# Performance work log

Hardware: AMD Instinct MI355X
Metric: run time of the kernel (lower is better)

Reference implementation:

```python
import jax, jax.numpy as jnp
import numpy as np

N_HEADS = 16
ROPE_THETA = 10000.0


def _rope(x):
    # x: (b, h, t, d). Interleaved-pair rotary embedding (lucidrains
    # rotary_embedding_torch convention: rotate_half on (d r) pairs, r=2).
    b, h, t, d = x.shape
    inv_freq = 1.0 / (ROPE_THETA ** (jnp.arange(0, d, 2, dtype=jnp.float32) / d))  # (d/2,)
    ang = jnp.arange(t, dtype=jnp.float32)[:, None] * inv_freq[None, :]            # (t, d/2)
    cos = jnp.cos(ang)
    sin = jnp.sin(ang)
    xp = x.reshape(b, h, t, d // 2, 2)
    x1, x2 = xp[..., 0], xp[..., 1]
    o1 = x1 * cos - x2 * sin
    o2 = x1 * sin + x2 * cos
    return jnp.stack([o1, o2], axis=-1).reshape(b, h, t, d)


def setup_inputs() -> dict:
    key = jax.random.key(0)
    k1, k2, k3 = jax.random.split(key, 3)
    B, T, C = 4, 2048, 1024
    x = jax.random.normal(k1, (B, T, C), dtype=jnp.float32)
    # torch nn.Linear weight layout: (out_features, in_features)
    w_attn = jax.random.normal(k2, (3 * C, C), dtype=jnp.float32) * (1.0 / np.sqrt(C))
    w_proj = jax.random.normal(k3, (C, C), dtype=jnp.float32) * (1.0 / np.sqrt(C))
    return {"x": x, "w_attn": w_attn, "w_proj": w_proj}


def reference(x, w_attn, w_proj):
    B, T, C = x.shape
    H = N_HEADS
    D = C // H
    # fused QKV projection: (b, t, 3C)
    qkv = jnp.einsum('btc,fc->btf', x, w_attn)
    # rearrange 'b t (r h d) -> r b h t d'
    qkv = qkv.reshape(B, T, 3, H, D).transpose(2, 0, 3, 1, 4)
    q, k, v = qkv[0], qkv[1], qkv[2]
    q = _rope(q)
    k = _rope(k)
    scale = 1.0 / np.sqrt(D).astype(np.float32)
    scores = jnp.einsum('bhqd,bhkd->bhqk', q, k) * scale
    attn = jax.nn.softmax(scores, axis=-1)
    y = jnp.einsum('bhqk,bhkd->bhqd', attn, v)       # (b, h, t, d)
    y = y.transpose(0, 2, 1, 3).reshape(B, T, C)     # 'b h t d -> b t (h d)'
    return jnp.einsum('btc,oc->bto', y, w_proj)
```

## Files before the change

kernel.cpp:

```cpp
#include <hip/hip_runtime.h>
#include <hip/hip_bf16.h>
#include <math.h>

typedef __bf16 bf16;
typedef float f32x4 __attribute__((ext_vector_type(4)));
typedef float f32x16 __attribute__((ext_vector_type(16)));
typedef bf16 bf16x8 __attribute__((ext_vector_type(8)));
typedef bf16 bf16x4 __attribute__((ext_vector_type(4)));
typedef unsigned int uint;
typedef uint uintx2 __attribute__((ext_vector_type(2)));

#define MFMA16(a, b, c) __builtin_amdgcn_mfma_f32_16x16x32_bf16(a, b, c, 0, 0, 0)
#define MFMA32(a, b, c) __builtin_amdgcn_mfma_f32_32x32x16_bf16(a, b, c, 0, 0, 0)

static constexpr int T_SEQ = 2048;
static constexpr int CDIM  = 1024;
static constexpr int NH    = 16;
static constexpr int DH    = 64;
static constexpr float FREQ_C = 0.20762050593045998f;
static constexpr float Q_SCALE = 0.18033688011112042f;

__device__ __forceinline__ float fexp2(float x) {
    return __builtin_amdgcn_exp2f(x);
}

__device__ __forceinline__ uint pack_bf16(float lo, float hi) {
    union { bf16 h[2]; uint u; } cv;
    cv.h[0] = (bf16)lo;
    cv.h[1] = (bf16)hi;
    return cv.u;
}

__device__ __forceinline__ void gld_lds16(const bf16* g, bf16* l) {
    __builtin_amdgcn_global_load_lds(
        (const __attribute__((address_space(1))) void*)g,
        (__attribute__((address_space(3))) void*)l, 16, 0, 0);
}

__device__ __forceinline__ void fast_sincos(float x, float* s, float* c) {
    const float INV2PI = 0.15915494309189535f;
    const float PI2_HI = 6.28125f;
    const float PI2_LO = 1.9353071795864769e-3f;
    const float n = rintf(x * INV2PI);
    float r = fmaf(-n, PI2_HI, x);
    r = fmaf(-n, PI2_LO, r);
    *s = __sinf(r);
    *c = __cosf(r);
}

__device__ __forceinline__ void cvt8(const float* __restrict__ in,
                                     bf16* __restrict__ out, int i) {
    const f32x4* p = (const f32x4*)(in + (size_t)i * 8);
    const f32x4 lo = p[0], hi = p[1];
    bf16x8 o;
    o[0] = (bf16)lo[0]; o[1] = (bf16)lo[1]; o[2] = (bf16)lo[2]; o[3] = (bf16)lo[3];
    o[4] = (bf16)hi[0]; o[5] = (bf16)hi[1]; o[6] = (bf16)hi[2]; o[7] = (bf16)hi[3];
    *(bf16x8*)(out + (size_t)i * 8) = o;
}

__global__ __launch_bounds__(256)
void prologue(const float* __restrict__ x, const float* __restrict__ wa,
              const float* __restrict__ wp, bf16* __restrict__ Xb,
              bf16* __restrict__ Wab, bf16* __restrict__ Wpb,
              float2* __restrict__ tab) {
    const int b = blockIdx.x, tid = threadIdx.x;
    if (b < 4096) {
        cvt8(x, Xb, b * 256 + tid);
    } else if (b < 5632) {
        cvt8(wa, Wab, (b - 4096) * 256 + tid);
    } else if (b < 6144) {
        cvt8(wp, Wpb, (b - 5632) * 256 + tid);
    } else {
        const int i = (b - 6144) * 256 + tid;
        const int t = i >> 5, p = i & 31;
        const float ang = (float)t * exp2f(-2.0f * (float)p * FREQ_C);
        float s, c;
        fast_sincos(ang, &s, &c);
        tab[i] = make_float2(c, s);
    }
}

#define GEMM_CORE(Abase, Bbase, KDIM)                                            \
    f32x4 acc[4][4] = {};                                                        \
    for (int kk = 0; kk < (KDIM); kk += 64) {                                    \
        __syncthreads();                                                         \
        _Pragma("unroll")                                                        \
        for (int u = 0; u < 4; u++) {                                            \
            const int st = wave * 4 + u, mg = st >> 1, kg = st & 1;              \
            gld_lds16(Abase + (size_t)(mg * 16 + sm) * (KDIM) + kk + kg * 32 + sc * 8, \
                      &ash[st * 512]);                                           \
            gld_lds16(Bbase + (size_t)(mg * 16 + sm) * (KDIM) + kk + kg * 32 + sc * 8, \
                      &bsh[st * 512]);                                           \
        }                                                                        \
        __syncthreads();                                                         \
        _Pragma("unroll")                                                        \
        for (int kg = 0; kg < 2; kg++) {                                         \
            bf16x8 af[4], bfr[4];                                                \
            _Pragma("unroll")                                                    \
            for (int a = 0; a < 4; a++)                                          \
                af[a] = *(const bf16x8*)&ash[((wm * 4 + a) * 2 + kg) * 512 + lane * 8]; \
            _Pragma("unroll")                                                    \
            for (int b = 0; b < 4; b++)                                          \
                bfr[b] = *(const bf16x8*)&bsh[((wn * 4 + b) * 2 + kg) * 512 + lane * 8]; \
            _Pragma("unroll")                                                    \
            for (int a = 0; a < 4; a++)                                          \
                _Pragma("unroll")                                                \
                for (int b = 0; b < 4; b++)                                      \
                    acc[a][b] = MFMA16(af[a], bfr[b], acc[a][b]);                \
        }                                                                        \
    }

__global__ __launch_bounds__(256)
void gemm_qkv(const bf16* __restrict__ X, const bf16* __restrict__ W,
              bf16* __restrict__ Qo, bf16* __restrict__ Ko, bf16* __restrict__ Vt,
              const float2* __restrict__ tab) {
    __shared__ __align__(16) bf16 ash[16 * 512];
    __shared__ __align__(16) bf16 bsh[16 * 512];
    const int tid = threadIdx.x, lane = tid & 63, wave = tid >> 6;
    const int quad = lane >> 4, l16 = lane & 15;
    const int wm = wave >> 1, wn = wave & 1;
    const int lin = blockIdx.y * 24 + blockIdx.x;
    const int xcd = lin & 7, j = lin >> 3;
    const int bm = xcd * 8 + (j & 7), bn = j >> 3;
    const int sm = lane & 15, sc = lane >> 4;

    const bf16* Abase = X + (size_t)(bm * 128) * CDIM;
    const bf16* Bbase = W + (size_t)(bn * 128) * CDIM;
    GEMM_CORE(Abase, Bbase, CDIM)

    const int rr    = (bn * 128) >> 10;
    const int nsec  = (bn * 128) & 1023;
    const int batch = (bm * 128) >> 11;
    const int tb    = ((bm * 128) & 2047) + wm * 64;

    if (rr == 2) {
#pragma unroll
        for (int b = 0; b < 4; b++) {
            const int n = nsec + wn * 64 + b * 16 + l16;
            const int h = n >> 6, d = n & 63;
            bf16* vp = Vt + ((size_t)(batch * NH + h) * DH + d) * T_SEQ;
#pragma unroll
            for (int a = 0; a < 4; a++) {
                const int t0 = tb + a * 16 + quad * 4;
                bf16x4 pk4 = { (bf16)acc[a][b][0], (bf16)acc[a][b][1],
                               (bf16)acc[a][b][2], (bf16)acc[a][b][3] };
                *(bf16x4*)(vp + t0) = pk4;
            }
        }
    } else {
        bf16* Dst = (rr == 0) ? Qo : Ko;
        const float scale = (rr == 0) ? Q_SCALE : 1.0f;
#pragma unroll
        for (int b = 0; b < 4; b++) {
            const int n = nsec + wn * 64 + b * 16 + l16;
            const int h = n >> 6, d = n & 63;
            const int p = d >> 1, odd = d & 1;
            bf16* dp = Dst + (size_t)(batch * NH + h) * T_SEQ * DH + d;
#pragma unroll
            for (int a = 0; a < 4; a++) {
#pragma unroll
                for (int r = 0; r < 4; r++) {
                    const int t = tb + a * 16 + quad * 4 + r;
                    const float val = acc[a][b][r];
                    const float partner = __shfl_xor(val, 1);
                    const float2 cs = tab[t * 32 + p];
                    float o = odd ? (partner * cs.y + val * cs.x)
                                  : (val * cs.x - partner * cs.y);
                    dp[(size_t)t * DH] = (bf16)(o * scale);
                }
            }
        }
    }
}

__global__ __launch_bounds__(256)
void gemm_proj(const bf16* __restrict__ X, const bf16* __restrict__ W,
               float* __restrict__ Out) {
    __shared__ __align__(16) bf16 ash[16 * 512];
    __shared__ __align__(16) bf16 bsh[16 * 512];
    const int tid = threadIdx.x, lane = tid & 63, wave = tid >> 6;
    const int quad = lane >> 4, l16 = lane & 15;
    const int wm = wave >> 1, wn = wave & 1;
    const int lin = blockIdx.y * 8 + blockIdx.x;
    const int xcd = lin & 7, j = lin >> 3;
    const int bm = xcd * 8 + (j & 7), bn = j >> 3;
    const int sm = lane & 15, sc = lane >> 4;

    const bf16* Abase = X + (size_t)(bm * 128) * CDIM;
    const bf16* Bbase = W + (size_t)(bn * 128) * CDIM;
    GEMM_CORE(Abase, Bbase, CDIM)

#pragma unroll
    for (int b = 0; b < 4; b++) {
        const int n = bn * 128 + wn * 64 + b * 16 + l16;
#pragma unroll
        for (int a = 0; a < 4; a++) {
            const int m = bm * 128 + wm * 64 + a * 16 + quad * 4;
#pragma unroll
            for (int r = 0; r < 4; r++)
                Out[(size_t)(m + r) * CDIM + n] = acc[a][b][r];
        }
    }
}

__global__ __launch_bounds__(256)
void flash(const bf16* __restrict__ Q, const bf16* __restrict__ K,
           const bf16* __restrict__ Vt, bf16* __restrict__ Y) {
    __shared__ __align__(16) bf16 ksh[2][8 * 512];
    __shared__ __align__(16) bf16 vsh[2][8 * 512];
    const int tid = threadIdx.x, lane = tid & 63, wave = tid >> 6;
    const int l32 = lane & 31, hi = lane >> 5;
    const int id = blockIdx.x;
    const int bh = (id & 7) * 8 + ((id >> 3) & 7);
    const int qsb = id >> 6;
    const size_t kbase = (size_t)bh * T_SEQ * DH;
    const size_t vbase = (size_t)bh * DH * T_SEQ;
    const int q0 = qsb * 256 + wave * 32;

    bf16x8 bq[2][4];
#pragma unroll
    for (int tq = 0; tq < 2; tq++) {
        const bf16* qp = Q + kbase + (size_t)(q0 + tq * 128 + l32) * DH + hi * 8;
#pragma unroll
        for (int c = 0; c < 4; c++) bq[tq][c] = *(const bf16x8*)(qp + c * 16);
    }

    f32x16 oT[2][2] = {};
    f32x16 lf[2] = {};
    bf16x8 onesf;
#pragma unroll
    for (int j = 0; j < 8; j++) onesf[j] = (bf16)1.0f;

#define STAGE(buf_, kt_) do {                                              \
        if (wave < 2) {                                                    \
            _Pragma("unroll")                                              \
            for (int u = 0; u < 4; u++) {                                  \
                const int s = wave * 4 + u, kb = s >> 2, c = s & 3;        \
                gld_lds16(K + kbase + (size_t)((kt_) + kb * 32 + l32) * DH \
                              + c * 16 + hi * 8,                           \
                          &ksh[buf_][s * 512]);                            \
            }                                                              \
        } else {                                                           \
            _Pragma("unroll")                                              \
            for (int u = 0; u < 4; u++) {                                  \
                const int s = (wave - 2) * 4 + u, db = s >> 2, kc = s & 3; \
                gld_lds16(Vt + vbase + (size_t)(db * 32 + l32) * T_SEQ     \
                              + (kt_) + kc * 16 + hi * 8,                  \
                          &vsh[buf_][s * 512]);                            \
            }                                                              \
        }                                                                  \
    } while (0)

    STAGE(0, 0);
    int ib = 0;
    for (int kt = 0; kt < T_SEQ; kt += 64, ib ^= 1) {
        __syncthreads();
        if (kt + 64 < T_SEQ) STAGE(ib ^ 1, kt + 64);

#pragma unroll
        for (int kb = 0; kb < 2; kb++) {
            f32x16 s0 = {}, s1 = {};
#pragma unroll
            for (int c = 0; c < 4; c++) {
                const bf16x8 a = *(const bf16x8*)&ksh[ib][(kb * 4 + c) * 512 + lane * 8];
                s0 = MFMA32(a, bq[0][c], s0);
                s1 = MFMA32(a, bq[1][c], s1);
            }
            uint P[2][8];
#pragma unroll
            for (int w = 0; w < 8; w++) {
                P[0][w] = pack_bf16(fexp2(s0[2 * w]), fexp2(s0[2 * w + 1]));
                P[1][w] = pack_bf16(fexp2(s1[2 * w]), fexp2(s1[2 * w + 1]));
            }
#pragma unroll
            for (int t = 0; t < 2; t++) {
                const int kc = kb * 2 + t;
                bf16x8 vv[2];
#pragma unroll
                for (int db = 0; db < 2; db++)
                    vv[db] = *(const bf16x8*)&vsh[ib][(db * 4 + kc) * 512 + lane * 8];
#pragma unroll
                for (int tq = 0; tq < 2; tq++) {
                    const uintx2 rA = __builtin_amdgcn_permlane32_swap(
                        P[tq][4 * t + 0], P[tq][4 * t + 2], false, false);
                    const uintx2 rB = __builtin_amdgcn_permlane32_swap(
                        P[tq][4 * t + 1], P[tq][4 * t + 3], false, false);
                    union { uint u[4]; bf16x8 v; } bP;
                    bP.u[0] = rA[0]; bP.u[1] = rB[0];
                    bP.u[2] = rA[1]; bP.u[3] = rB[1];
                    lf[tq] = MFMA32(onesf, bP.v, lf[tq]);
#pragma unroll
                    for (int db = 0; db < 2; db++)
                        oT[tq][db] = MFMA32(vv[db], bP.v, oT[tq][db]);
                }
            }
        }
    }
#undef STAGE

    const int b = bh >> 4, h = bh & 15;
#pragma unroll
    for (int tq = 0; tq < 2; tq++) {
        const float inv = 1.0f / lf[tq][0];
        const size_t yrow =
            ((size_t)b * T_SEQ + q0 + tq * 128 + l32) * CDIM + h * DH;
#pragma unroll
        for (int db = 0; db < 2; db++)
#pragma unroll
            for (int rg = 0; rg < 4; rg++) {
                bf16x4 o4 = { (bf16)(oT[tq][db][rg * 4 + 0] * inv),
                              (bf16)(oT[tq][db][rg * 4 + 1] * inv),
                              (bf16)(oT[tq][db][rg * 4 + 2] * inv),
                              (bf16)(oT[tq][db][rg * 4 + 3] * inv) };
                *(bf16x4*)(Y + yrow + db * 32 + 8 * rg + 4 * hi) = o4;
            }
    }
}

extern "C" void kernel_launch(void* const* d_in, const int* in_sizes, int n_in,
                              void* d_out, int out_size, void* d_ws, size_t ws_size,
                              hipStream_t stream) {
    const float* x      = (const float*)d_in[0];
    const float* w_attn = (const float*)d_in[1];
    const float* w_proj = (const float*)d_in[2];
    float* out = (float*)d_out;

    bf16* ws = (bf16*)d_ws;
    const size_t SZ = (size_t)4 * NH * T_SEQ * DH;
    bf16* Xb  = ws;
    bf16* Wab = Xb + SZ;
    bf16* Wpb = Wab + 3145728;
    bf16* Qb  = Wpb + 1048576;
    bf16* Kb  = Qb + SZ;
    bf16* Vtb = Kb + SZ;
    bf16* Yb  = Vtb + SZ;
    float2* tab = (float2*)(Yb + SZ);

    prologue<<<6400, 256, 0, stream>>>(x, w_attn, w_proj, Xb, Wab, Wpb, tab);
    gemm_qkv<<<dim3(24, 64), 256, 0, stream>>>(Xb, Wab, Qb, Kb, Vtb, tab);
    flash<<<512, 256, 0, stream>>>(Qb, Kb, Vtb, Yb);
    gemm_proj<<<dim3(8, 64), 256, 0, stream>>>(Yb, Wpb, out);
}
```

Before: 318.6 us.

## Rewrite QKV GEMM as 256x256 double-buffered tile with 8 waves

The QKV projection GEMM moves from 128x128 tiles with 4 waves and a single LDS buffer to 256x256 tiles with 8 waves (512 threads), double-buffered LDS, and the next k-slice prefetched while MFMAs run. It also raises wave priority around the MFMA blocks and uses explicit barriers and sched_barriers. The goals are more data reuse per tile and hiding global-to-LDS latency. In exchange it uses 128 KB of LDS per block and more registers, which limits occupancy, and the grid shrinks to 384 blocks, which may leave the 256 CUs unevenly loaded.

```diff
diff --git a/kernel.cpp b/kernel.cpp
--- a/kernel.cpp
+++ b/kernel.cpp
@@ -77,6 +77,121 @@
         float s, c;
         fast_sincos(ang, &s, &c);
         tab[i] = make_float2(c, s);
+    }
+}
+
+__global__ __launch_bounds__(512, 2)
+void gemm_qkv(const bf16* __restrict__ X, const bf16* __restrict__ W,
+              bf16* __restrict__ Qo, bf16* __restrict__ Ko, bf16* __restrict__ Vt,
+              const float2* __restrict__ tab) {
+    __shared__ __align__(16) bf16 ash[2][32 * 512];
+    __shared__ __align__(16) bf16 bsh[2][32 * 512];
+    const int tid = threadIdx.x, lane = tid & 63, wave = tid >> 6;
+    const int quad = lane >> 4, l16 = lane & 15;
+    const int wm = wave >> 2, wn = wave & 3;
+    const int sm = lane & 15, sc = lane >> 4;
+    const int lin = blockIdx.y * 12 + blockIdx.x;
+    const int xcd = lin & 7, j = lin >> 3;
+    const int bmp = xcd * 4 + (j & 3), bnp = j >> 2;
+
+    const bf16* Abase = X + (size_t)(bmp * 256) * CDIM;
+    const bf16* Bbase = W + (size_t)(bnp * 256) * CDIM;
+
+    f32x4 acc[8][4] = {};
+
+#pragma unroll
+    for (int u = 0; u < 4; u++) {
+        const int st = wave * 4 + u, mg = st >> 1, kg = st & 1;
+        const size_t off = (size_t)(mg * 16 + sm) * CDIM + kg * 32 + sc * 8;
+        gld_lds16(Abase + off, &ash[0][st * 512]);
+        gld_lds16(Bbase + off, &bsh[0][st * 512]);
+    }
+
+    for (int t = 0; t < 16; t++) {
+        const int buf = t & 1;
+        bf16x8 af[8];
+#pragma unroll
+        for (int q = 0; q < 4; q++) {
+            const int kg = q >> 1, bp = q & 1;
+            if (q == 0) asm volatile("s_waitcnt vmcnt(0)" ::: "memory");
+            __builtin_amdgcn_s_barrier();
+            __builtin_amdgcn_sched_barrier(0);
+            if (bp == 0) {
+#pragma unroll
+                for (int a = 0; a < 8; a++)
+                    af[a] = *(const bf16x8*)
+                        &ash[buf][((wm * 8 + a) * 2 + kg) * 512 + lane * 8];
+            }
+            bf16x8 bfr[2];
+#pragma unroll
+            for (int bb = 0; bb < 2; bb++)
+                bfr[bb] = *(const bf16x8*)
+                    &bsh[buf][((wn * 4 + bp * 2 + bb) * 2 + kg) * 512 + lane * 8];
+            if (q < 2 && t + 1 < 16) {
+#pragma unroll
+                for (int v = 0; v < 2; v++) {
+                    const int st = wave * 4 + q * 2 + v, mg = st >> 1, kg2 = st & 1;
+                    const size_t off = (size_t)(mg * 16 + sm) * CDIM
+                                       + (t + 1) * 64 + kg2 * 32 + sc * 8;
+                    gld_lds16(Abase + off, &ash[buf ^ 1][st * 512]);
+                    gld_lds16(Bbase + off, &bsh[buf ^ 1][st * 512]);
+                }
+            }
+            __builtin_amdgcn_sched_barrier(0);
+            __builtin_amdgcn_s_setprio(1);
+#pragma unroll
+            for (int a = 0; a < 8; a++)
+#pragma unroll
+                for (int bb = 0; bb < 2; bb++)
+                    acc[a][bp * 2 + bb] =
+                        MFMA16(af[a], bfr[bb], acc[a][bp * 2 + bb]);
+            __builtin_amdgcn_s_setprio(0);
+        }
+    }
+
+    const int colbase = bnp * 256 + wn * 64;
+    const int rr    = colbase >> 10;
+    const int nsec  = colbase & 1023;
+    const int batch = (bmp * 256) >> 11;
+    const int tb    = ((bmp * 256) & 2047) + wm * 128;
+
+    if (rr == 2) {
+#pragma unroll
+        for (int b = 0; b < 4; b++) {
+            const int n = nsec + b * 16 + l16;
+            const int h = n >> 6, d = n & 63;
+            bf16* vp = Vt + ((size_t)(batch * NH + h) * DH + d) * T_SEQ;
+#pragma unroll
+            for (int a = 0; a < 8; a++) {
+                const int t0 = tb + a * 16 + quad * 4;
+                bf16x4 pk4 = { (bf16)acc[a][b][0], (bf16)acc[a][b][1],
+                               (bf16)acc[a][b][2], (bf16)acc[a][b][3] };
+                *(bf16x4*)(vp + t0) = pk4;
+            }
+        }
+    } else {
+        bf16* Dst = (rr == 0) ? Qo : Ko;
+        const float scale = (rr == 0) ? Q_SCALE : 1.0f;
+#pragma unroll
+        for (int b = 0; b < 4; b++) {
+            const int n = nsec + b * 16 + l16;
+            const int h = n >> 6, d = n & 63;
+            const int p = d >> 1, odd = d & 1;
+            bf16* dp = Dst + (size_t)(batch * NH + h) * T_SEQ * DH + d;
+#pragma unroll
+            for (int a = 0; a < 8; a++) {
+#pragma unroll
+                for (int r = 0; r < 4; r++) {
+                    const int trow = tb + a * 16 + quad * 4 + r;
+                    const float val = acc[a][b][r];
+                    const float partner = __shfl_xor(val, 1);
+                    const float2 cs = tab[trow * 32 + p];
+                    float o = odd ? (partner * cs.y + val * cs.x)
+                                  : (val * cs.x - partner * cs.y);
+                    dp[(size_t)trow * DH] = (bf16)(o * scale);
+                }
+            }
+        }
     }
 }
 
@@ -111,69 +226,6 @@
     }
 
 __global__ __launch_bounds__(256)
-void gemm_qkv(const bf16* __restrict__ X, const bf16* __restrict__ W,
-              bf16* __restrict__ Qo, bf16* __restrict__ Ko, bf16* __restrict__ Vt,
-              const float2* __restrict__ tab) {
-    __shared__ __align__(16) bf16 ash[16 * 512];
-    __shared__ __align__(16) bf16 bsh[16 * 512];
-    const int tid = threadIdx.x, lane = tid & 63, wave = tid >> 6;
-    const int quad = lane >> 4, l16 = lane & 15;
-    const int wm = wave >> 1, wn = wave & 1;
-    const int lin = blockIdx.y * 24 + blockIdx.x;
-    const int xcd = lin & 7, j = lin >> 3;
-    const int bm = xcd * 8 + (j & 7), bn = j >> 3;
-    const int sm = lane & 15, sc = lane >> 4;
-
-    const bf16* Abase = X + (size_t)(bm * 128) * CDIM;
-    const bf16* Bbase = W + (size_t)(bn * 128) * CDIM;
-    GEMM_CORE(Abase, Bbase, CDIM)
-
-    const int rr    = (bn * 128) >> 10;
-    const int nsec  = (bn * 128) & 1023;
-    const int batch = (bm * 128) >> 11;
-    const int tb    = ((bm * 128) & 2047) + wm * 64;
-
-    if (rr == 2) {
-#pragma unroll
-        for (int b = 0; b < 4; b++) {
-            const int n = nsec + wn * 64 + b * 16 + l16;
-            const int h = n >> 6, d = n & 63;
-            bf16* vp = Vt + ((size_t)(batch * NH + h) * DH + d) * T_SEQ;
-#pragma unroll
-            for (int a = 0; a < 4; a++) {
-                const int t0 = tb + a * 16 + quad * 4;
-                bf16x4 pk4 = { (bf16)acc[a][b][0], (bf16)acc[a][b][1],
-                               (bf16)acc[a][b][2], (bf16)acc[a][b][3] };
-                *(bf16x4*)(vp + t0) = pk4;
-            }
-        }
-    } else {
-        bf16* Dst = (rr == 0) ? Qo : Ko;
-        const float scale = (rr == 0) ? Q_SCALE : 1.0f;
-#pragma unroll
-        for (int b = 0; b < 4; b++) {
-            const int n = nsec + wn * 64 + b * 16 + l16;
-            const int h = n >> 6, d = n & 63;
-            const int p = d >> 1, odd = d & 1;
-            bf16* dp = Dst + (size_t)(batch * NH + h) * T_SEQ * DH + d;
-#pragma unroll
-            for (int a = 0; a < 4; a++) {
-#pragma unroll
-                for (int r = 0; r < 4; r++) {
-                    const int t = tb + a * 16 + quad * 4 + r;
-                    const float val = acc[a][b][r];
-                    const float partner = __shfl_xor(val, 1);
-                    const float2 cs = tab[t * 32 + p];
-                    float o = odd ? (partner * cs.y + val * cs.x)
-                                  : (val * cs.x - partner * cs.y);
-                    dp[(size_t)t * DH] = (bf16)(o * scale);
-                }
-            }
-        }
-    }
-}
-
-__global__ __launch_bounds__(256)
 void gemm_proj(const bf16* __restrict__ X, const bf16* __restrict__ W,
                float* __restrict__ Out) {
     __shared__ __align__(16) bf16 ash[16 * 512];
@@ -337,7 +389,7 @@
     float2* tab = (float2*)(Yb + SZ);
 
     prologue<<<6400, 256, 0, stream>>>(x, w_attn, w_proj, Xb, Wab, Wpb, tab);
-    gemm_qkv<<<dim3(24, 64), 256, 0, stream>>>(Xb, Wab, Qb, Kb, Vtb, tab);
+    gemm_qkv<<<dim3(12, 32), 512, 0, stream>>>(Xb, Wab, Qb, Kb, Vtb, tab);
     flash<<<512, 256, 0, stream>>>(Qb, Kb, Vtb, Yb);
     gemm_proj<<<dim3(8, 64), 256, 0, stream>>>(Yb, Wpb, out);
 }
```

After: 323.1 us. No clear change (+1.4%).

## Load K/V fragments directly from global and compute row sums with scalar adds

Applied to the files above, without the earlier changes.

The flash kernel no longer stages K and V tiles through double-buffered LDS with barriers. Each wave now loads its own K and V fragments straight from global memory into registers. The softmax denominator moves from an MFMA against a ones vector to scalar float accumulation, with a cross-half shuffle at the end. This removes LDS traffic, __syncthreads and one MFMA per chunk. In exchange, every wave re-reads the same K/V from global/L2 (four times the traffic), there is no software prefetch overlap, and register pressure rises.

```diff
diff --git a/kernel.cpp b/kernel.cpp
--- a/kernel.cpp
+++ b/kernel.cpp
@@ -206,8 +206,6 @@
 __global__ __launch_bounds__(256)
 void flash(const bf16* __restrict__ Q, const bf16* __restrict__ K,
            const bf16* __restrict__ Vt, bf16* __restrict__ Y) {
-    __shared__ __align__(16) bf16 ksh[2][8 * 512];
-    __shared__ __align__(16) bf16 vsh[2][8 * 512];
     const int tid = threadIdx.x, lane = tid & 63, wave = tid >> 6;
     const int l32 = lane & 31, hi = lane >> 5;
     const int id = blockIdx.x;
@@ -226,59 +224,47 @@
     }
 
     f32x16 oT[2][2] = {};
-    f32x16 lf[2] = {};
-    bf16x8 onesf;
-#pragma unroll
-    for (int j = 0; j < 8; j++) onesf[j] = (bf16)1.0f;
-
-#define STAGE(buf_, kt_) do {                                              \
-        if (wave < 2) {                                                    \
-            _Pragma("unroll")                                              \
-            for (int u = 0; u < 4; u++) {                                  \
-                const int s = wave * 4 + u, kb = s >> 2, c = s & 3;        \
-                gld_lds16(K + kbase + (size_t)((kt_) + kb * 32 + l32) * DH \
-                              + c * 16 + hi * 8,                           \
-                          &ksh[buf_][s * 512]);                            \
-            }                                                              \
-        } else {                                                           \
-            _Pragma("unroll")                                              \
-            for (int u = 0; u < 4; u++) {                                  \
-                const int s = (wave - 2) * 4 + u, db = s >> 2, kc = s & 3; \
-                gld_lds16(Vt + vbase + (size_t)(db * 32 + l32) * T_SEQ     \
-                              + (kt_) + kc * 16 + hi * 8,                  \
-                          &vsh[buf_][s * 512]);                            \
-            }                                                              \
-        }                                                                  \
-    } while (0)
-
-    STAGE(0, 0);
-    int ib = 0;
-    for (int kt = 0; kt < T_SEQ; kt += 64, ib ^= 1) {
-        __syncthreads();
-        if (kt + 64 < T_SEQ) STAGE(ib ^ 1, kt + 64);
+    float li[2] = {0.f, 0.f};
+
+    const bf16* kp = K + kbase + hi * 8;
+    const bf16* vp0 = Vt + vbase + (size_t)l32 * T_SEQ + hi * 8;
+    const bf16* vp1 = vp0 + (size_t)32 * T_SEQ;
+
+    for (int kt = 0; kt < T_SEQ; kt += 64) {
+        bf16x8 kf[8], vf[8];
+#pragma unroll
+        for (int i = 0; i < 8; i++) {
+            const int kb = i >> 2, c = i & 3;
+            kf[i] = *(const bf16x8*)(kp + (size_t)(kt + kb * 32 + l32) * DH + c * 16);
+        }
+#pragma unroll
+        for (int i = 0; i < 8; i++) {
+            const int db = i >> 2, kc = i & 3;
+            const bf16* vp = db ? vp1 : vp0;
+            vf[i] = *(const bf16x8*)(vp + kt + kc * 16);
+        }
 
 #pragma unroll
         for (int kb = 0; kb < 2; kb++) {
             f32x16 s0 = {}, s1 = {};
 #pragma unroll
             for (int c = 0; c < 4; c++) {
-                const bf16x8 a = *(const bf16x8*)&ksh[ib][(kb * 4 + c) * 512 + lane * 8];
-                s0 = MFMA32(a, bq[0][c], s0);
-                s1 = MFMA32(a, bq[1][c], s1);
+                s0 = MFMA32(kf[kb * 4 + c], bq[0][c], s0);
+                s1 = MFMA32(kf[kb * 4 + c], bq[1][c], s1);
             }
             uint P[2][8];
 #pragma unroll
             for (int w = 0; w < 8; w++) {
-                P[0][w] = pack_bf16(fexp2(s0[2 * w]), fexp2(s0[2 * w + 1]));
-                P[1][w] = pack_bf16(fexp2(s1[2 * w]), fexp2(s1[2 * w + 1]));
+                const float a0 = fexp2(s0[2 * w]), a1 = fexp2(s0[2 * w + 1]);
+                const float b0 = fexp2(s1[2 * w]), b1 = fexp2(s1[2 * w + 1]);
+                li[0] += a0 + a1;
+                li[1] += b0 + b1;
+                P[0][w] = pack_bf16(a0, a1);
+                P[1][w] = pack_bf16(b0, b1);
             }
 #pragma unroll
             for (int t = 0; t < 2; t++) {
                 const int kc = kb * 2 + t;
-                bf16x8 vv[2];
-#pragma unroll
-                for (int db = 0; db < 2; db++)
-                    vv[db] = *(const bf16x8*)&vsh[ib][(db * 4 + kc) * 512 + lane * 8];
 #pragma unroll
                 for (int tq = 0; tq < 2; tq++) {
                     const uintx2 rA = __builtin_amdgcn_permlane32_swap(
@@ -288,20 +274,19 @@
                     union { uint u[4]; bf16x8 v; } bP;
                     bP.u[0] = rA[0]; bP.u[1] = rB[0];
                     bP.u[2] = rA[1]; bP.u[3] = rB[1];
-                    lf[tq] = MFMA32(onesf, bP.v, lf[tq]);
 #pragma unroll
                     for (int db = 0; db < 2; db++)
-                        oT[tq][db] = MFMA32(vv[db], bP.v, oT[tq][db]);
+                        oT[tq][db] = MFMA32(vf[db * 4 + kc], bP.v, oT[tq][db]);
                 }
             }
         }
     }
-#undef STAGE
 
     const int b = bh >> 4, h = bh & 15;
 #pragma unroll
     for (int tq = 0; tq < 2; tq++) {
-        const float inv = 1.0f / lf[tq][0];
+        const float lsum = li[tq] + __shfl_xor(li[tq], 32);
+        const float inv = 1.0f / lsum;
         const size_t yrow =
             ((size_t)b * T_SEQ + q0 + tq * 128 + l32) * CDIM + h * DH;
 #pragma unroll
```

Measured after the change: 363.3 us. +14.0%, slower.
